# Optimization experiments

Measured on AMD Instinct MI355X. Metric: run time of the kernel, lower is better.

## Reference

```python
import jax, jax.numpy as jnp
import numpy as np

B, FEAT_DIM, GUIDE_DIM, NIR = 1, 128, 128, 33
HL, WL, HH, WH = 64, 64, 256, 256


def make_coord(h, w):
    # pixel-center coords in [-1,1], order (y, x) matching torch make_coord((h,w))
    ys = -1.0 + 1.0 / h + (2.0 / h) * jnp.arange(h, dtype=jnp.float32)
    xs = -1.0 + 1.0 / w + (2.0 / w) * jnp.arange(w, dtype=jnp.float32)
    yy, xx = jnp.meshgrid(ys, xs, indexing='ij')
    return jnp.stack([yy, xx], axis=-1)  # [h, w, 2]


def grid_sample_nearest(img, coord):
    # img [B,C,Hi,Wi]; coord [B,N,2] normalized (y,x).
    # Matches F.grid_sample(mode='nearest', align_corners=False, padding_mode='zeros')
    # (torch passes coord.flip(-1), i.e. (x,y); we index (y,x) directly -- equivalent).
    Bb, C, Hi, Wi = img.shape
    y, x = coord[..., 0], coord[..., 1]
    iy = jnp.round((y + 1.0) * Hi / 2.0 - 0.5).astype(jnp.int32)
    ix = jnp.round((x + 1.0) * Wi / 2.0 - 0.5).astype(jnp.int32)
    valid = (iy >= 0) & (iy < Hi) & (ix >= 0) & (ix < Wi)
    idx = jnp.clip(iy, 0, Hi - 1) * Wi + jnp.clip(ix, 0, Wi - 1)  # [B,N]
    g = jnp.take_along_axis(img.reshape(Bb, C, Hi * Wi), idx[:, None, :], axis=2)
    g = jnp.where(valid[:, None, :], g, 0.0)
    return jnp.transpose(g, (0, 2, 1))  # [B,N,C]


def depthwise3x3(x, k):
    C = x.shape[1]
    return jax.lax.conv_general_dilated(x, k[:, None, :, :], (1, 1), ((1, 1), (1, 1)),
                                        feature_group_count=C,
                                        dimension_numbers=('NCHW', 'OIHW', 'NCHW'))


def query_freq(feat, coord, hr_guide, mlp_fn):
    # local-ensemble implicit decode (query_freq_a / query_freq_p share this skeleton)
    b, c, h, w = feat.shape
    H, W = hr_guide.shape[-2], hr_guide.shape[-1]
    coord = jnp.broadcast_to(coord, (b, H * W, 2))
    fcoord = jnp.broadcast_to(jnp.transpose(make_coord(h, w), (2, 0, 1))[None], (b, 2, h, w))
    q_guide = grid_sample_nearest(hr_guide, coord)  # [b,N,Cg]
    rx, ry = 1.0 / h, 1.0 / w
    hw = jnp.array([float(h), float(w)], dtype=coord.dtype)
    preds = []
    for vx in (-1.0, 1.0):
        for vy in (-1.0, 1.0):
            c_ = coord + jnp.array([vx * rx, vy * ry], dtype=coord.dtype)
            q_feat = grid_sample_nearest(feat, c_)    # [b,N,Cf]
            q_coord = grid_sample_nearest(fcoord, c_)  # [b,N,2]
            rel = (coord - q_coord) * hw
            inp = jnp.concatenate([q_feat, q_guide, rel], axis=-1)  # [b,N,Cin]
            preds.append(mlp_fn(inp, H, W))  # [b,N,NIR]
    preds = jnp.stack(preds, axis=-1)  # [b,N,NIR,4]
    weight = jax.nn.softmax(preds[:, :, -1, :], axis=-1)  # [b,N,4]
    ret = jnp.sum(preds[:, :, :-1, :] * weight[:, :, None, :], axis=-1)  # [b,N,NIR-1]
    return jnp.transpose(ret, (0, 2, 1)).reshape(b, -1, H, W)


def fourier_unit(feat, coord, hr_guide, w1a, b1a, w2a, b2a, w3a, b3a,
                 pw1, dw1, pw2, dw2, pw3, dw3):
    def mlp_a(inp, H, W):  # plain MLP (imnet1)
        x = jax.nn.relu(inp @ w1a + b1a)
        x = jax.nn.relu(x @ w2a + b2a)
        return x @ w3a + b3a

    def mlp_p(inp, H, W):  # conv MLP (imnet2 / MLP_P)
        b = inp.shape[0]
        x = inp.reshape(b, -1, H, W)  # faithful to torch .view on [B,N,Cin]
        x = jax.nn.relu(depthwise3x3(jnp.einsum('bchw,oc->bohw', x, pw1), dw1))
        x = jax.nn.relu(depthwise3x3(jnp.einsum('bchw,oc->bohw', x, pw2), dw2))
        x = depthwise3x3(jnp.einsum('bchw,oc->bohw', x, pw3), dw3)
        return x.reshape(b, H * W, -1)  # faithful to torch .view(B,N,-1)

    feat_f = jnp.fft.fftn(feat, axes=(-2, -1))
    guide_f = jnp.fft.fftn(hr_guide, axes=(-2, -1))
    mag = query_freq(jnp.abs(feat_f), coord, jnp.abs(guide_f), mlp_a)
    pha = query_freq(jnp.angle(feat_f), coord, jnp.angle(guide_f), mlp_p)
    ffted = jax.lax.complex(mag * jnp.cos(pha), mag * jnp.sin(pha))
    return jnp.abs(jnp.fft.ifftn(ffted, axes=(-2, -1)))


def setup_inputs() -> dict:
    key = jax.random.key(0)
    ks = jax.random.split(key, 12)
    cin = FEAT_DIM + GUIDE_DIM + 2  # 258

    def lin(k, i, o):
        return jax.random.normal(k, (i, o), jnp.float32) / np.float32(np.sqrt(i))

    return dict(
        feat=jax.random.normal(ks[0], (B, FEAT_DIM, HL, WL), jnp.float32),
        coord=make_coord(HH, WH).reshape(1, HH * WH, 2),
        hr_guide=jax.random.normal(ks[1], (B, GUIDE_DIM, HH, WH), jnp.float32),
        w1a=lin(ks[2], cin, 256), b1a=jnp.zeros((256,), jnp.float32),
        w2a=lin(ks[3], 256, 128), b2a=jnp.zeros((128,), jnp.float32),
        w3a=lin(ks[4], 128, NIR), b3a=jnp.zeros((NIR,), jnp.float32),
        pw1=jax.random.normal(ks[5], (256, cin), jnp.float32) / np.float32(np.sqrt(cin)),
        dw1=jax.random.normal(ks[6], (256, 3, 3), jnp.float32) / np.float32(3.0),
        pw2=jax.random.normal(ks[7], (128, 256), jnp.float32) / np.float32(16.0),
        dw2=jax.random.normal(ks[8], (128, 3, 3), jnp.float32) / np.float32(3.0),
        pw3=jax.random.normal(ks[9], (NIR, 128), jnp.float32) / np.float32(np.sqrt(128.0)),
        dw3=jax.random.normal(ks[10], (NIR, 3, 3), jnp.float32) / np.float32(3.0),
    )


def reference(feat, coord, hr_guide, w1a, b1a, w2a, b2a, w3a, b3a,
              pw1, dw1, pw2, dw2, pw3, dw3):
    return fourier_unit(feat, coord, hr_guide, w1a, b1a, w2a, b2a, w3a, b3a,
                        pw1, dw1, pw2, dw2, pw3, dw3)
```

## Files before the change

kernel.cpp:

```cpp
#include <hip/hip_runtime.h>
#include <math.h>

typedef __attribute__((ext_vector_type(4))) float f32x4;
typedef __attribute__((ext_vector_type(8))) short bf16x8;
typedef _Float16 f16x8 __attribute__((ext_vector_type(8)));

__device__ __forceinline__ short f2bf(float v) {
    union { float f; unsigned u; } x; x.f = v;
    unsigned r = x.u + 0x7FFF + ((x.u >> 16) & 1);
    return (short)(r >> 16);
}
__device__ __forceinline__ float bf2f(short b) {
    union { unsigned u; float f; } x; x.u = ((unsigned)(unsigned short)b) << 16;
    return x.f;
}
__device__ __forceinline__ short f2h(float v) {
    union { _Float16 h; short s; } u; u.h = (_Float16)v; return u.s;
}
__device__ __forceinline__ void gload16(const void* g, void* l) {
    __builtin_amdgcn_global_load_lds((const __attribute__((address_space(1))) void*)g,
                                     (__attribute__((address_space(3))) void*)l, 16, 0, 0);
}

template<int N, int MODE>
__global__ __launch_bounds__(256)
void fft_lines(const float* __restrict__ in_real, const float* __restrict__ in_pha,
               const float2* __restrict__ in_c, float2* __restrict__ out_c,
               int nlines, int lpp, int plane_stride, int line_pitch, int stride,
               float sgn, float scale)
{
    constexpr int H = N / 2;
    constexpr int LPB = 256 / H;
    __shared__ float2 bufA[LPB][N];
    __shared__ float2 bufB[LPB][N];
    __shared__ float2 W[H];
    const int tid = threadIdx.x;
    const int sub = tid / H;
    const int b   = tid % H;
    const int L   = blockIdx.x * LPB + sub;
    if (tid < H) {
        float ang = (6.283185307179586f / N) * tid;
        float s, c; sincosf(ang, &s, &c);
        W[tid] = make_float2(c, sgn * s);
    }
    const bool active = (L < nlines);
    size_t base = 0;
    if (active) {
        int p = L / lpp, q = L - p * lpp;
        base = (size_t)p * plane_stride + (size_t)q * line_pitch;
        if (MODE == 0) {
            bufA[sub][b]     = make_float2(in_real[base + (size_t)b * stride], 0.f);
            bufA[sub][b + H] = make_float2(in_real[base + (size_t)(b + H) * stride], 0.f);
        } else if (MODE == 1) {
            bufA[sub][b]     = in_c[base + (size_t)b * stride];
            bufA[sub][b + H] = in_c[base + (size_t)(b + H) * stride];
        } else {
            float m0 = in_real[base + (size_t)b * stride];
            float p0 = in_pha [base + (size_t)b * stride];
            float m1 = in_real[base + (size_t)(b + H) * stride];
            float p1 = in_pha [base + (size_t)(b + H) * stride];
            float s0, c0, s1, c1;
            sincosf(p0, &s0, &c0);
            sincosf(p1, &s1, &c1);
            bufA[sub][b]     = make_float2(m0 * c0, m0 * s0);
            bufA[sub][b + H] = make_float2(m1 * c1, m1 * s1);
        }
    }
    __syncthreads();
    float2 (*X)[N] = bufA;
    float2 (*Y)[N] = bufB;
    int m = 1;
    #pragma unroll
    for (int l = H; l >= 1; l >>= 1) {
        int jm = b & ~(m - 1);
        float2 c0 = X[sub][b];
        float2 c1 = X[sub][b + H];
        float2 w  = W[jm];
        float2 s0 = make_float2(c0.x + c1.x, c0.y + c1.y);
        float2 d  = make_float2(c0.x - c1.x, c0.y - c1.y);
        float2 t  = make_float2(d.x * w.x - d.y * w.y, d.x * w.y + d.y * w.x);
        Y[sub][b + jm]     = s0;
        Y[sub][b + jm + m] = t;
        __syncthreads();
        float2 (*tmp)[N] = X; X = Y; Y = tmp;
        m <<= 1;
    }
    if (active) {
        float2 r0 = X[sub][b], r1 = X[sub][b + H];
        out_c[base + (size_t)b * stride]       = make_float2(r0.x * scale, r0.y * scale);
        out_c[base + (size_t)(b + H) * stride] = make_float2(r1.x * scale, r1.y * scale);
    }
}

template<int N, int TC, int ABSOUT>
__global__ __launch_bounds__(256)
void fft_cols(const float2* __restrict__ in, float2* __restrict__ outc,
              float* __restrict__ outr, float sgn, float scale)
{
    constexpr int Q     = N / 4;
    constexpr int LOG4  = (N == 64) ? 3 : 4;
    constexpr int PITCH = ((N + N / 8 - 8 + 31) / 32) * 32 + 8;
    constexpr int ELD   = (N * TC) / 256;
    constexpr int EBF   = (Q * TC) / 256;
    static_assert((Q * TC) % 256 == 0, "butterfly count must fill block");
    __shared__ float bRe[2][TC * PITCH];
    __shared__ float bIm[2][TC * PITCH];
    __shared__ float Wre[Q + Q / 8 + 1];
    __shared__ float Wim[Q + Q / 8 + 1];
    const int tid = threadIdx.x;
    const int plane = blockIdx.y;
    const int c0 = blockIdx.x * TC;
    const size_t pbase = (size_t)plane * N * N + c0;
    auto lidx = [](int cc, int row) { return cc * PITCH + row + (row >> 3); };

    if (tid < Q) {
        float ang = (6.283185307179586f / N) * tid;
        float s, c; sincosf(ang, &s, &c);
        int wi = tid + (tid >> 3);
        Wre[wi] = c; Wim[wi] = sgn * s;
    }
    #pragma unroll
    for (int e = 0; e < ELD; e++) {
        int q = tid + e * 256;
        int r = q / TC, cc = q % TC;
        float2 v = in[pbase + (size_t)r * N + cc];
        int li = lidx(cc, r);
        bRe[0][li] = v.x; bIm[0][li] = v.y;
    }
    __syncthreads();
    int cur = 0, m = 1;
    #pragma unroll
    for (int stage = 0; stage < LOG4; stage++) {
        #pragma unroll
        for (int e = 0; e < EBF; e++) {
            int idx = tid + e * 256;
            int b = idx % Q, cc = idx / Q;
            int jm = b & ~(m - 1);
            int base = 3 * jm + b;
            int i0 = lidx(cc, b),         i1 = lidx(cc, b + Q);
            int i2 = lidx(cc, b + 2 * Q), i3 = lidx(cc, b + 3 * Q);
            float x0r = bRe[cur][i0], x0i = bIm[cur][i0];
            float x1r = bRe[cur][i1], x1i = bIm[cur][i1];
            float x2r = bRe[cur][i2], x2i = bIm[cur][i2];
            float x3r = bRe[cur][i3], x3i = bIm[cur][i3];
            int wi = jm + (jm >> 3);
            float w1r = Wre[wi], w1i = Wim[wi];
            float w2r = w1r * w1r - w1i * w1i, w2i = 2.f * w1r * w1i;
            float w3r = w2r * w1r - w2i * w1i, w3i = w2r * w1i + w2i * w1r;
            float ar = x0r + x2r, ai = x0i + x2i;
            float br = x0r - x2r, bi = x0i - x2i;
            float cr = x1r + x3r, ci = x1i + x3i;
            float dr = x1r - x3r, di = x1i - x3i;
            float edr = -sgn * di, edi = sgn * dr;
            float y0r = ar + cr,  y0i = ai + ci;
            float y1r = br + edr, y1i = bi + edi;
            float y2r = ar - cr,  y2i = ai - ci;
            float y3r = br - edr, y3i = bi - edi;
            int o0 = lidx(cc, base),         o1 = lidx(cc, base + m);
            int o2 = lidx(cc, base + 2 * m), o3 = lidx(cc, base + 3 * m);
            bRe[cur ^ 1][o0] = y0r;                     bIm[cur ^ 1][o0] = y0i;
            bRe[cur ^ 1][o1] = y1r * w1r - y1i * w1i;   bIm[cur ^ 1][o1] = y1r * w1i + y1i * w1r;
            bRe[cur ^ 1][o2] = y2r * w2r - y2i * w2i;   bIm[cur ^ 1][o2] = y2r * w2i + y2i * w2r;
            bRe[cur ^ 1][o3] = y3r * w3r - y3i * w3i;   bIm[cur ^ 1][o3] = y3r * w3i + y3i * w3r;
        }
        __syncthreads();
        cur ^= 1; m <<= 2;
    }
    #pragma unroll
    for (int e = 0; e < ELD; e++) {
        int q = tid + e * 256;
        int r = q / TC, cc = q % TC;
        int li = lidx(cc, r);
        float vr = bRe[cur][li], vi = bIm[cur][li];
        if (ABSOUT) {
            outr[pbase + (size_t)r * N + cc] = scale * sqrtf(vr * vr + vi * vi);
        } else {
            outc[pbase + (size_t)r * N + cc] = make_float2(vr * scale, vi * scale);
        }
    }
}

__global__ __launch_bounds__(256)
void extract_t(const float2* __restrict__ Fc, short* __restrict__ fAbf,
               float* __restrict__ fPT)
{
    __shared__ float2 T[128][17];
    const int tid = threadIdx.x;
    const int o0 = blockIdx.x * 16;
    #pragma unroll
    for (int e = 0; e < 8; e++) {
        int q = tid + e * 256;
        int c = q >> 4, oo = q & 15;
        T[c][oo] = Fc[(size_t)c * 4096 + o0 + oo];
    }
    __syncthreads();
    #pragma unroll
    for (int e = 0; e < 8; e++) {
        int q = tid + e * 256;
        int oo = q >> 7, c = q & 127;
        float2 v = T[c][oo];
        size_t idx = (size_t)(o0 + oo) * 128 + c;
        fAbf[idx] = f2bf(sqrtf(v.x * v.x + v.y * v.y));
        fPT[idx]  = atan2f(v.y, v.x);
    }
}

__global__ __launch_bounds__(256)
void gbuild_t(const float2* __restrict__ E, short* __restrict__ Ga,
              float* __restrict__ Gpf)
{
    __shared__ float2 T[128][17];
    const int tid = threadIdx.x;
    const int n0 = blockIdx.x * 16;
    #pragma unroll
    for (int e = 0; e < 8; e++) {
        int q = tid + e * 256;
        int c = q >> 4, nn = q & 15;
        T[c][nn] = E[(size_t)c * 65536 + n0 + nn];
    }
    __syncthreads();
    #pragma unroll
    for (int e = 0; e < 8; e++) {
        int q = tid + e * 256;
        int nn = q >> 7, c = q & 127;
        float2 v = T[c][nn];
        size_t o = (size_t)(n0 + nn) * 128 + c;
        Ga[o]  = f2bf(sqrtf(v.x * v.x + v.y * v.y));
        Gpf[o] = atan2f(v.y, v.x);
    }
}

__global__ __launch_bounds__(256)
void mag_h1(const short* __restrict__ FA1, const short* __restrict__ H1g,
            const float* __restrict__ w1a, const float* __restrict__ b1a,
            short* __restrict__ h1, int vx, int vy)
{
    int t = blockIdx.x * 256 + threadIdx.x;
    int n = t >> 5, oc = (t & 31) * 8;
    int i = n >> 8, jx = n & 255;
    int iy = (2 * i + (vx < 0 ? -3 : 5)) >> 3;
    int ix = (2 * jx + (vy < 0 ? -3 : 5)) >> 3;
    bool valid = (iy >= 0 && iy < 64 && ix >= 0 && ix < 64);
    float ry = valid ? (0.5f * i - 2.f * iy - 0.75f) : (0.5f * i - 63.75f);
    float rx = valid ? (0.5f * jx - 2.f * ix - 0.75f) : (0.5f * jx - 63.75f);
    bf16x8 hv = *(const bf16x8*)&H1g[(size_t)n * 256 + oc];
    bf16x8 fv = {};
    if (valid) fv = *(const bf16x8*)&FA1[(size_t)(iy * 64 + ix) * 256 + oc];
    bf16x8 out;
    #pragma unroll
    for (int k = 0; k < 8; k++) {
        int o = oc + k;
        float v = b1a[o] + bf2f(hv[k]) + ry * w1a[128 * 256 + o] + rx * w1a[129 * 256 + o];
        if (valid) v += bf2f(fv[k]);
        out[k] = f2bf(fmaxf(v, 0.f));
    }
    *(bf16x8*)&h1[(size_t)n * 256 + oc] = out;
}

__global__ __launch_bounds__(256)
void bphase_tile(const float* __restrict__ featPT, const float* __restrict__ Gpf,
                 short* __restrict__ Xp, int vx, int vy)
{
    __shared__ short lds[64 * 146];
    const int tid = threadIdx.x;
    const int p0 = (blockIdx.x >> 1) * 64;
    const int half = blockIdx.x & 1;
    const int pl = tid & 63;
    const int p = p0 + pl;
    const int jq = tid >> 6;
    unsigned* out32 = (unsigned*)Xp;
    #pragma unroll 4
    for (int e = 0; e < 36; e++) {
        int jl = e * 4 + jq;
        int j = half * 144 + jl;
        float v = 0.f;
        if (j < 258) {
            unsigned f = (unsigned)j * 65536u + (unsigned)p;
            unsigned n = f / 258u;
            unsigned c = f - n * 258u;
            int i = (int)(n >> 8), jx = (int)(n & 255);
            int iy = (2 * i + (vx < 0 ? -3 : 5)) >> 3;
            int ix = (2 * jx + (vy < 0 ? -3 : 5)) >> 3;
            bool valid = (iy >= 0 && iy < 64 && ix >= 0 && ix < 64);
            if (c < 128u)       v = valid ? featPT[(size_t)(iy * 64 + ix) * 128 + c] : 0.f;
            else if (c < 256u)  v = Gpf[(size_t)n * 128 + (c - 128)];
            else if (c == 256u) v = valid ? (0.5f * i - 2.f * iy - 0.75f) : (0.5f * i - 63.75f);
            else                v = valid ? (0.5f * jx - 2.f * ix - 0.75f) : (0.5f * jx - 63.75f);
        }
        lds[pl * 146 + jl] = f2h(v);
    }
    __syncthreads();
    const unsigned* lds32 = (const unsigned*)lds;
    #pragma unroll 4
    for (int e = 0; e < 18; e++) {
        int idx = e * 256 + tid;
        int pw = idx / 72, dw = idx - pw * 72;
        out32[(size_t)(p0 + pw) * 144 + half * 72 + dw] = lds32[pw * 73 + dw];
    }
}

__global__ void wprep_T(const float* __restrict__ src, short* __restrict__ dst,
                        int Ncols, int Nd, int Kp, int k0, int kn, int kr0, int krn)
{
    int t = blockIdx.x * 256 + threadIdx.x;
    if (t >= Nd * Kp) return;
    int o = t / Kp, j = t - o * Kp;
    int c = (j < kn) ? (k0 + j) : ((j < kn + krn) ? (kr0 + j - kn) : -1);
    float v = 0.f;
    if (c >= 0 && o < Ncols) v = src[(size_t)c * Ncols + o];
    dst[t] = f2bf(v);
}
__global__ void wprep_f16(const float* __restrict__ src, short* __restrict__ dst,
                          int Nsrc, int Ksrc, int Nd, int Kp, int kn)
{
    int t = blockIdx.x * 256 + threadIdx.x;
    if (t >= Nd * Kp) return;
    int o = t / Kp, j = t - o * Kp;
    float v = 0.f;
    if (j < kn && o < Nsrc) v = src[(size_t)o * Ksrc + j];
    dst[t] = f2h(v);
}

template<int RELU, int BIAS, int CIN, int OUTT, int F16>
__global__ __launch_bounds__(256)
void gemm_mfma(const short* __restrict__ A, const short* __restrict__ Bt,
               const float* __restrict__ bias, const void* __restrict__ Cin,
               void* __restrict__ Cout,
               int K, int Apitch, int Bpitch, int ldc, int Nout)
{
    __shared__ short As[4096];
    __shared__ short Bs[4096];
    const int tid = threadIdx.x;
    const int wave = tid >> 6, lane = tid & 63;
    const int bm = blockIdx.y * 128, bn = blockIdx.x * 128;
    const int wr = wave >> 1, wc = wave & 1;
    const int srow = wave * 32 + (lane >> 2);
    const int scol = (lane & 3) * 8;
    const int ldsoff = srow * 32 + scol;
    f32x4 acc[4][4] = {};
    const int ks_n = K >> 5;
    for (int ks = 0; ks < ks_n; ks++) {
        const int k0 = ks << 5;
        const short* gA = A + (size_t)(bm + srow) * Apitch + k0 + scol;
        gload16(gA, &As[ldsoff]);
        gload16(gA + 16 * Apitch, &As[ldsoff + 512]);
        const short* gB = Bt + (size_t)(bn + srow) * Bpitch + k0 + scol;
        gload16(gB, &Bs[ldsoff]);
        gload16(gB + 16 * Bpitch, &Bs[ldsoff + 512]);
        __syncthreads();
        const int fr = lane & 15;
        const int kreg = (lane >> 4) << 3;
        bf16x8 ah[4], bh[4];
        #pragma unroll
        for (int m = 0; m < 4; m++)
            ah[m] = *(const bf16x8*)&As[(wr * 64 + m * 16 + fr) * 32 + kreg];
        #pragma unroll
        for (int n = 0; n < 4; n++)
            bh[n] = *(const bf16x8*)&Bs[(wc * 64 + n * 16 + fr) * 32 + kreg];
        #pragma unroll
        for (int m = 0; m < 4; m++)
            #pragma unroll
            for (int n = 0; n < 4; n++) {
                if constexpr (F16)
                    acc[m][n] = __builtin_amdgcn_mfma_f32_16x16x32_f16(
                        __builtin_bit_cast(f16x8, ah[m]),
                        __builtin_bit_cast(f16x8, bh[n]), acc[m][n], 0, 0, 0);
                else
                    acc[m][n] = __builtin_amdgcn_mfma_f32_16x16x32_bf16(
                        ah[m], bh[n], acc[m][n], 0, 0, 0);
            }
        __syncthreads();
    }
    const int fr = lane & 15;
    const int rg = (lane >> 4) * 4;
    #pragma unroll
    for (int n = 0; n < 4; n++) {
        const int col = bn + wc * 64 + n * 16 + fr;
        if (col >= Nout) continue;
        const float bv = BIAS ? bias[col] : 0.f;
        #pragma unroll
        for (int m = 0; m < 4; m++) {
            const int row0 = bm + wr * 64 + m * 16 + rg;
            #pragma unroll
            for (int r = 0; r < 4; r++) {
                float v = acc[m][n][r] + bv;
                const size_t ci = (size_t)(row0 + r) * ldc + col;
                if (CIN == 1) v += bf2f(((const short*)Cin)[ci]);
                if (RELU) v = fmaxf(v, 0.f);
                if constexpr (OUTT == 1)      ((float*)Cout)[ci] = v;
                else if constexpr (OUTT == 2) ((_Float16*)Cout)[ci] = (_Float16)v;
                else                          ((short*)Cout)[ci] = f2bf(v);
            }
        }
    }
}

template<int C, int RELU>
__global__ __launch_bounds__(256)
void dwconv_f16(const _Float16* __restrict__ in, const float* __restrict__ w,
                _Float16* __restrict__ out)
{
    constexpr int PX = 512 / C;
    const int tid = threadIdx.x;
    const int c = tid % C;
    const int sub = tid / C;
    const int p0 = blockIdx.x * PX + sub * 2;
    const int y = p0 >> 8, x0 = p0 & 255;
    float wk[9];
    #pragma unroll
    for (int k = 0; k < 9; k++) wk[k] = w[c * 9 + k];
    float v[3][4];
    #pragma unroll
    for (int dy = 0; dy < 3; dy++) {
        int yy = y + dy - 1;
        bool yv = (yy >= 0) && (yy <= 255);
        int yc = min(max(yy, 0), 255);
        #pragma unroll
        for (int dx = 0; dx < 4; dx++) {
            int xx = x0 + dx - 1;
            bool xv = (xx >= 0) && (xx <= 255);
            int xc = min(max(xx, 0), 255);
            float t = (float)in[(size_t)(yc * 256 + xc) * C + c];
            v[dy][dx] = (yv && xv) ? t : 0.f;
        }
    }
    float a0 = 0.f, a1 = 0.f;
    #pragma unroll
    for (int dy = 0; dy < 3; dy++)
        #pragma unroll
        for (int dx = 0; dx < 3; dx++) {
            a0 += v[dy][dx]     * wk[dy * 3 + dx];
            a1 += v[dy][dx + 1] * wk[dy * 3 + dx];
        }
    if (RELU) { a0 = fmaxf(a0, 0.f); a1 = fmaxf(a1, 0.f); }
    out[(size_t)p0 * C + c]       = (_Float16)a0;
    out[(size_t)(p0 + 1) * C + c] = (_Float16)a1;
}

__global__ __launch_bounds__(256)
void dwconv3_t(const float* __restrict__ in, const float* __restrict__ w,
               float* __restrict__ out)
{
    __shared__ float lds[33][65];
    const int tid = threadIdx.x;
    const int y = blockIdx.x >> 2;
    const int x0 = (blockIdx.x & 3) * 64;
    #pragma unroll
    for (int e = 0; e < 9; e++) {
        int q = e * 256 + tid;
        if (q < 2112) {
            int x = q / 33, c = q - x * 33;
            float acc = 0.f;
            #pragma unroll
            for (int dy = 0; dy < 3; dy++) {
                int yy = y + dy - 1;
                bool yv = (yy >= 0) && (yy <= 255);
                int yc = min(max(yy, 0), 255);
                #pragma unroll
                for (int dx = 0; dx < 3; dx++) {
                    int xx = x0 + x + dx - 1;
                    bool xv = (xx >= 0) && (xx <= 255);
                    int xc = min(max(xx, 0), 255);
                    float t = in[(size_t)(yc * 256 + xc) * 33 + c];
                    acc += ((yv && xv) ? t : 0.f) * w[c * 9 + dy * 3 + dx];
                }
            }
            lds[c][x] = acc;
        }
    }
    __syncthreads();
    const int xx = tid & 63, c4 = tid >> 6;
    #pragma unroll
    for (int cg = 0; cg < 36; cg += 4) {
        int cc = cg + c4;
        if (cc < 33)
            out[(size_t)cc * 65536 + y * 256 + x0 + xx] = lds[cc][xx];
    }
}

__global__ __launch_bounds__(256)
void ensemble_a(const short* __restrict__ P, float* __restrict__ mag)
{
    int n = blockIdx.x * 256 + threadIdx.x;
    float w[4]; float mx = -1e30f;
    #pragma unroll
    for (int s = 0; s < 4; s++) {
        w[s] = bf2f(P[((size_t)s * 65536 + n) * 33 + 32]);
        mx = fmaxf(mx, w[s]);
    }
    float sum = 0.f;
    #pragma unroll
    for (int s = 0; s < 4; s++) { w[s] = expf(w[s] - mx); sum += w[s]; }
    float inv = 1.f / sum;
    for (int ch = 0; ch < 32; ch++) {
        float a = 0.f;
        #pragma unroll
        for (int s = 0; s < 4; s++)
            a += bf2f(P[((size_t)s * 65536 + n) * 33 + ch]) * w[s];
        mag[(size_t)ch * 65536 + n] = a * inv;
    }
}

__global__ __launch_bounds__(256)
void ensemble_p(const float* __restrict__ P, float* __restrict__ pha)
{
    const size_t SOFF = (size_t)65536 * 33;
    int n = blockIdx.x * 256 + threadIdx.x;
    const size_t base = (size_t)n * 33;
    float w[4]; float mx = -1e30f;
    #pragma unroll
    for (int s = 0; s < 4; s++) {
        w[s] = P[(size_t)s * SOFF + base + 32];
        mx = fmaxf(mx, w[s]);
    }
    float sum = 0.f;
    #pragma unroll
    for (int s = 0; s < 4; s++) { w[s] = expf(w[s] - mx); sum += w[s]; }
    float inv = 1.f / sum;
    for (int jj = 0; jj < 32; jj++) {
        float a = 0.f;
        #pragma unroll
        for (int s = 0; s < 4; s++)
            a += P[(size_t)s * SOFF + base + jj] * w[s];
        pha[(size_t)jj * 65536 + n] = a * inv;
    }
}

extern "C" void kernel_launch(void* const* d_in, const int* in_sizes, int n_in,
                              void* d_out, int out_size, void* d_ws, size_t ws_size,
                              hipStream_t stream)
{
    (void)in_sizes; (void)n_in; (void)out_size; (void)ws_size;
    const float* feat = (const float*)d_in[0];
    const float* hr   = (const float*)d_in[2];
    const float* w1a  = (const float*)d_in[3];
    const float* b1a  = (const float*)d_in[4];
    const float* w2a  = (const float*)d_in[5];
    const float* b2a  = (const float*)d_in[6];
    const float* w3a  = (const float*)d_in[7];
    const float* b3a  = (const float*)d_in[8];
    const float* pw1  = (const float*)d_in[9];
    const float* dw1  = (const float*)d_in[10];
    const float* pw2  = (const float*)d_in[11];
    const float* dw2  = (const float*)d_in[12];
    const float* pw3  = (const float*)d_in[13];
    const float* dw3  = (const float*)d_in[14];

    char* W = (char*)d_ws;
    const size_t oA = 0;
    const size_t oB = 75497472;
    const size_t oC = oB + 67108864;
    const size_t oD = oC + 33554432;
    const size_t oM = oD + 34603008;
    const size_t oF = oM + 12582912;
    const size_t oN = oF + 786432;

    float2* E    = (float2*)(W + oA);
    short*  Xp   = (short*) (W + oA);
    _Float16* X2 = (_Float16*)(W + oA);
    short*  h1   = (short*) (W + oA + 20971520);
    float*  C3   = (float*) (W + oA);
    float*  Hp   = (float*) (W + oA);
    float2* Fc   = (float2*)(W + oB);
    short*  Ga   = (short*) (W + oB);
    short*  H1g  = (short*) (W + oB + 16777216);
    short*  h2   = (short*) (W + oB + 50331648);
    _Float16* C1 = (_Float16*)(W + oB);
    _Float16* C2 = (_Float16*)(W + oB);
    _Float16* X3 = (_Float16*)(W + oB + 33554432);
    float2* Z    = (float2*)(W + oB);
    float*  Gpf  = (float*) (W + oC);
    short*  PA   = (short*) (W + oD);
    float*  PP   = (float*) (W + oD);
    float*  featPT = (float*)(W + oM);
    float*  Hm     = (float*)(W + oM + 4194304);
    short* W1g = (short*)(W + oF + 81920);
    short* W2  = (short*)(W + oF + 147456);
    short* W3  = (short*)(W + oF + 212992);
    short* Pf  = (short*)(W + oF + 245760);
    short* P2  = (short*)(W + oF + 393216);
    short* P3  = (short*)(W + oF + 458752);
    short* W1a128 = (short*)(W + oF + 491520);
    short* featAbf = (short*)(W + oN);
    short* FA1     = (short*)(W + oN + 1048576);

    const size_t SOFF = (size_t)65536 * 33;

    wprep_T<<<128, 256, 0, stream>>>(w1a, W1a128, 256, 256, 128, 0, 128, 0, 0);
    wprep_T<<<128, 256, 0, stream>>>(w1a, W1g, 256, 256, 128, 128, 128, 0, 0);
    wprep_T<<<128, 256, 0, stream>>>(w2a, W2, 128, 128, 256, 0, 256, 0, 0);
    wprep_T<<<64,  256, 0, stream>>>(w3a, W3, 33, 128, 128, 0, 128, 0, 0);
    wprep_f16<<<288, 256, 0, stream>>>(pw1, Pf, 256, 258, 256, 288, 258);
    wprep_f16<<<128, 256, 0, stream>>>(pw2, P2, 128, 256, 128, 256, 256);
    wprep_f16<<<64,  256, 0, stream>>>(pw3, P3, 33, 128, 128, 128, 128);

    fft_lines<256, 0><<<16384, 256, 0, stream>>>(hr, nullptr, nullptr, E, 32768, 256, 65536, 256, 1, -1.f, 1.f);
    fft_cols<256, 8, 0><<<dim3(32, 128), 256, 0, stream>>>(E, E, nullptr, -1.f, 1.f);
    fft_lines<64, 0><<<1024, 256, 0, stream>>>(feat, nullptr, nullptr, Fc, 8192, 64, 4096, 64, 1, -1.f, 1.f);
    fft_cols<64, 16, 0><<<dim3(4, 128), 256, 0, stream>>>(Fc, Fc, nullptr, -1.f, 1.f);
    extract_t<<<256, 256, 0, stream>>>(Fc, featAbf, featPT);

    gbuild_t<<<4096, 256, 0, stream>>>(E, Ga, Gpf);

    gemm_mfma<0,0,0,0,0><<<dim3(2,512), 256, 0, stream>>>(Ga, W1g, nullptr, nullptr, H1g, 128, 128, 128, 256, 256);
    gemm_mfma<0,0,0,0,0><<<dim3(2,32), 256, 0, stream>>>(featAbf, W1a128, nullptr, nullptr, FA1, 128, 128, 128, 256, 256);

    for (int s = 0; s < 4; s++) {
        int vx = (s < 2) ? -1 : 1;
        int vy = (s & 1) ? 1 : -1;
        mag_h1<<<8192, 256, 0, stream>>>(FA1, H1g, w1a, b1a, h1, vx, vy);
        gemm_mfma<1,1,0,0,0><<<dim3(1,512), 256, 0, stream>>>(h1, W2, b2a, nullptr, h2, 256, 256, 256, 128, 128);
        gemm_mfma<0,1,0,0,0><<<dim3(1,512), 256, 0, stream>>>(h2, W3, b3a, nullptr, PA + (size_t)s * 65536 * 33, 128, 128, 128, 33, 33);
    }
    ensemble_a<<<256, 256, 0, stream>>>(PA, Hm);

    for (int s = 0; s < 4; s++) {
        int vx = (s < 2) ? -1 : 1;
        int vy = (s & 1) ? 1 : -1;
        bphase_tile<<<2048, 256, 0, stream>>>(featPT, Gpf, Xp, vx, vy);
        gemm_mfma<0,0,0,2,1><<<dim3(2,512), 256, 0, stream>>>(Xp, Pf, nullptr, nullptr, C1, 288, 288, 288, 256, 256);
        dwconv_f16<256,1><<<32768, 256, 0, stream>>>(C1, dw1, X2);
        gemm_mfma<0,0,0,2,1><<<dim3(1,512), 256, 0, stream>>>((const short*)X2, P2, nullptr, nullptr, C2, 256, 256, 256, 128, 128);
        dwconv_f16<128,1><<<16384, 256, 0, stream>>>(C2, dw2, X3);
        gemm_mfma<0,0,0,1,1><<<dim3(1,512), 256, 0, stream>>>((const short*)X3, P3, nullptr, nullptr, C3, 128, 128, 128, 33, 33);
        dwconv3_t<<<1024, 256, 0, stream>>>(C3, dw3, PP + (size_t)s * SOFF);
    }
    ensemble_p<<<256, 256, 0, stream>>>(PP, Hp);

    fft_lines<256, 2><<<4096, 256, 0, stream>>>(Hm, Hp, nullptr, Z, 8192, 256, 65536, 256, 1, 1.f, 1.f / 256.f);
    fft_cols<256, 8, 1><<<dim3(32, 32), 256, 0, stream>>>(Z, nullptr, (float*)d_out, 1.f, 1.f / 256.f);
}
```

Measured before the change: 838.3 us.

## Batch two ensemble shifts per launch in amplitude and phase pipelines

The four per-shift kernel chains now run as two iterations, each covering two shifts, with grids doubled and kernels deriving the shift from the block or pixel index. The aim is fewer launches and larger grids that fill the GPU better, cutting launch gaps and tail effects. Intermediate buffers are relaid out so they hold two shifts at once, which raises the working-set size and memory footprint and adds aliasing risk in the scratch buffer.

```diff
diff --git a/kernel.cpp b/kernel.cpp
--- a/kernel.cpp
+++ b/kernel.cpp
@@ -233,17 +233,21 @@
 __global__ __launch_bounds__(256)
 void mag_h1(const short* __restrict__ FA1, const short* __restrict__ H1g,
             const float* __restrict__ w1a, const float* __restrict__ b1a,
-            short* __restrict__ h1, int vx, int vy)
+            short* __restrict__ h1, int s0)
 {
     int t = blockIdx.x * 256 + threadIdx.x;
     int n = t >> 5, oc = (t & 31) * 8;
-    int i = n >> 8, jx = n & 255;
-    int iy = (2 * i + (vx < 0 ? -3 : 5)) >> 3;
-    int ix = (2 * jx + (vy < 0 ? -3 : 5)) >> 3;
+    int im = n >> 16, nl = n & 65535;
+    int s = s0 + im;
+    int oy = (s < 2) ? -3 : 5;
+    int ox = (s & 1) ? 5 : -3;
+    int i = nl >> 8, jx = nl & 255;
+    int iy = (2 * i + oy) >> 3;
+    int ix = (2 * jx + ox) >> 3;
     bool valid = (iy >= 0 && iy < 64 && ix >= 0 && ix < 64);
     float ry = valid ? (0.5f * i - 2.f * iy - 0.75f) : (0.5f * i - 63.75f);
     float rx = valid ? (0.5f * jx - 2.f * ix - 0.75f) : (0.5f * jx - 63.75f);
-    bf16x8 hv = *(const bf16x8*)&H1g[(size_t)n * 256 + oc];
+    bf16x8 hv = *(const bf16x8*)&H1g[(size_t)nl * 256 + oc];
     bf16x8 fv = {};
     if (valid) fv = *(const bf16x8*)&FA1[(size_t)(iy * 64 + ix) * 256 + oc];
     bf16x8 out;
@@ -259,16 +263,21 @@
 
 __global__ __launch_bounds__(256)
 void bphase_tile(const float* __restrict__ featPT, const float* __restrict__ Gpf,
-                 short* __restrict__ Xp, int vx, int vy)
+                 short* __restrict__ Xp, int s0)
 {
     __shared__ short lds[64 * 146];
     const int tid = threadIdx.x;
-    const int p0 = (blockIdx.x >> 1) * 64;
-    const int half = blockIdx.x & 1;
+    const int sh = blockIdx.x >> 11;
+    const int inner = blockIdx.x & 2047;
+    const int s = s0 + sh;
+    const int oy = (s < 2) ? -3 : 5;
+    const int ox = (s & 1) ? 5 : -3;
+    const int p0 = (inner >> 1) * 64;
+    const int half = inner & 1;
     const int pl = tid & 63;
     const int p = p0 + pl;
     const int jq = tid >> 6;
-    unsigned* out32 = (unsigned*)Xp;
+    unsigned* out32 = (unsigned*)Xp + (size_t)sh * 65536 * 144;
     #pragma unroll 4
     for (int e = 0; e < 36; e++) {
         int jl = e * 4 + jq;
@@ -279,8 +288,8 @@
             unsigned n = f / 258u;
             unsigned c = f - n * 258u;
             int i = (int)(n >> 8), jx = (int)(n & 255);
-            int iy = (2 * i + (vx < 0 ? -3 : 5)) >> 3;
-            int ix = (2 * jx + (vy < 0 ? -3 : 5)) >> 3;
+            int iy = (2 * i + oy) >> 3;
+            int ix = (2 * jx + ox) >> 3;
             bool valid = (iy >= 0 && iy < 64 && ix >= 0 && ix < 64);
             if (c < 128u)       v = valid ? featPT[(size_t)(iy * 64 + ix) * 128 + c] : 0.f;
             else if (c < 256u)  v = Gpf[(size_t)n * 128 + (c - 128)];
@@ -405,7 +414,10 @@
     const int c = tid % C;
     const int sub = tid / C;
     const int p0 = blockIdx.x * PX + sub * 2;
-    const int y = p0 >> 8, x0 = p0 & 255;
+    const int im = p0 >> 16;
+    const int pl = p0 & 65535;
+    const int y = pl >> 8, x0 = pl & 255;
+    const size_t ibase = (size_t)im * 65536 * C;
     float wk[9];
     #pragma unroll
     for (int k = 0; k < 9; k++) wk[k] = w[c * 9 + k];
@@ -420,7 +432,7 @@
             int xx = x0 + dx - 1;
             bool xv = (xx >= 0) && (xx <= 255);
             int xc = min(max(xx, 0), 255);
-            float t = (float)in[(size_t)(yc * 256 + xc) * C + c];
+            float t = (float)in[ibase + (size_t)(yc * 256 + xc) * C + c];
             v[dy][dx] = (yv && xv) ? t : 0.f;
         }
     }
@@ -443,8 +455,12 @@
 {
     __shared__ float lds[33][65];
     const int tid = threadIdx.x;
-    const int y = blockIdx.x >> 2;
-    const int x0 = (blockIdx.x & 3) * 64;
+    const int im = blockIdx.x >> 10;
+    const int inner = blockIdx.x & 1023;
+    const int y = inner >> 2;
+    const int x0 = (inner & 3) * 64;
+    const size_t ibase = (size_t)im * 65536 * 33;
+    const size_t obase = (size_t)im * 65536 * 33;
     #pragma unroll
     for (int e = 0; e < 9; e++) {
         int q = e * 256 + tid;
@@ -461,7 +477,7 @@
                     int xx = x0 + x + dx - 1;
                     bool xv = (xx >= 0) && (xx <= 255);
                     int xc = min(max(xx, 0), 255);
-                    float t = in[(size_t)(yc * 256 + xc) * 33 + c];
+                    float t = in[ibase + (size_t)(yc * 256 + xc) * 33 + c];
                     acc += ((yv && xv) ? t : 0.f) * w[c * 9 + dy * 3 + dx];
                 }
             }
@@ -474,7 +490,7 @@
     for (int cg = 0; cg < 36; cg += 4) {
         int cc = cg + c4;
         if (cc < 33)
-            out[(size_t)cc * 65536 + y * 256 + x0 + xx] = lds[cc][xx];
+            out[obase + (size_t)cc * 65536 + y * 256 + x0 + xx] = lds[cc][xx];
     }
 }
 
@@ -555,23 +571,23 @@
     const size_t oF = oM + 12582912;
     const size_t oN = oF + 786432;
 
-    float2* E    = (float2*)(W + oA);
-    short*  Xp   = (short*) (W + oA);
-    _Float16* X2 = (_Float16*)(W + oA);
-    short*  h1   = (short*) (W + oA + 20971520);
-    float*  C3   = (float*) (W + oA);
-    float*  Hp   = (float*) (W + oA);
-    float2* Fc   = (float2*)(W + oB);
-    short*  Ga   = (short*) (W + oB);
-    short*  H1g  = (short*) (W + oB + 16777216);
-    short*  h2   = (short*) (W + oB + 50331648);
-    _Float16* C1 = (_Float16*)(W + oB);
-    _Float16* C2 = (_Float16*)(W + oB);
-    _Float16* X3 = (_Float16*)(W + oB + 33554432);
-    float2* Z    = (float2*)(W + oB);
-    float*  Gpf  = (float*) (W + oC);
-    short*  PA   = (short*) (W + oD);
-    float*  PP   = (float*) (W + oD);
+    float2* E     = (float2*)(W + oA);
+    short*  h1_2  = (short*) (W + oA);
+    short*  Xp2   = (short*) (W + oA);
+    _Float16* X2_2 = (_Float16*)(W + oA);
+    float*  C3_2  = (float*) (W + oA);
+    float*  Hp    = (float*) (W + oA);
+    float2* Fc    = (float2*)(W + oB);
+    short*  Ga    = (short*) (W + oB);
+    short*  h2_2  = (short*) (W + oB);
+    short*  H1g   = (short*) (W + oB + 33554432);
+    _Float16* C1_2 = (_Float16*)(W + oB);
+    _Float16* C2_2 = (_Float16*)(W + oB);
+    _Float16* X3_2 = (_Float16*)(W + oB + 33554432);
+    float2* Z     = (float2*)(W + oB);
+    float*  Gpf   = (float*) (W + oC);
+    short*  PA    = (short*) (W + oD);
+    float*  PP    = (float*) (W + oD);
     float*  featPT = (float*)(W + oM);
     float*  Hm     = (float*)(W + oM + 4194304);
     short* W1g = (short*)(W + oF + 81920);
@@ -605,25 +621,21 @@
     gemm_mfma<0,0,0,0,0><<<dim3(2,512), 256, 0, stream>>>(Ga, W1g, nullptr, nullptr, H1g, 128, 128, 128, 256, 256);
     gemm_mfma<0,0,0,0,0><<<dim3(2,32), 256, 0, stream>>>(featAbf, W1a128, nullptr, nullptr, FA1, 128, 128, 128, 256, 256);
 
-    for (int s = 0; s < 4; s++) {
-        int vx = (s < 2) ? -1 : 1;
-        int vy = (s & 1) ? 1 : -1;
-        mag_h1<<<8192, 256, 0, stream>>>(FA1, H1g, w1a, b1a, h1, vx, vy);
-        gemm_mfma<1,1,0,0,0><<<dim3(1,512), 256, 0, stream>>>(h1, W2, b2a, nullptr, h2, 256, 256, 256, 128, 128);
-        gemm_mfma<0,1,0,0,0><<<dim3(1,512), 256, 0, stream>>>(h2, W3, b3a, nullptr, PA + (size_t)s * 65536 * 33, 128, 128, 128, 33, 33);
+    for (int s0 = 0; s0 < 4; s0 += 2) {
+        mag_h1<<<16384, 256, 0, stream>>>(FA1, H1g, w1a, b1a, h1_2, s0);
+        gemm_mfma<1,1,0,0,0><<<dim3(1,1024), 256, 0, stream>>>(h1_2, W2, b2a, nullptr, h2_2, 256, 256, 256, 128, 128);
+        gemm_mfma<0,1,0,0,0><<<dim3(1,1024), 256, 0, stream>>>(h2_2, W3, b3a, nullptr, PA + (size_t)s0 * SOFF, 128, 128, 128, 33, 33);
     }
     ensemble_a<<<256, 256, 0, stream>>>(PA, Hm);
 
-    for (int s = 0; s < 4; s++) {
-        int vx = (s < 2) ? -1 : 1;
-        int vy = (s & 1) ? 1 : -1;
-        bphase_tile<<<2048, 256, 0, stream>>>(featPT, Gpf, Xp, vx, vy);
-        gemm_mfma<0,0,0,2,1><<<dim3(2,512), 256, 0, stream>>>(Xp, Pf, nullptr, nullptr, C1, 288, 288, 288, 256, 256);
-        dwconv_f16<256,1><<<32768, 256, 0, stream>>>(C1, dw1, X2);
-        gemm_mfma<0,0,0,2,1><<<dim3(1,512), 256, 0, stream>>>((const short*)X2, P2, nullptr, nullptr, C2, 256, 256, 256, 128, 128);
-        dwconv_f16<128,1><<<16384, 256, 0, stream>>>(C2, dw2, X3);
-        gemm_mfma<0,0,0,1,1><<<dim3(1,512), 256, 0, stream>>>((const short*)X3, P3, nullptr, nullptr, C3, 128, 128, 128, 33, 33);
-        dwconv3_t<<<1024, 256, 0, stream>>>(C3, dw3, PP + (size_t)s * SOFF);
+    for (int s0 = 0; s0 < 4; s0 += 2) {
+        bphase_tile<<<4096, 256, 0, stream>>>(featPT, Gpf, Xp2, s0);
+        gemm_mfma<0,0,0,2,1><<<dim3(2,1024), 256, 0, stream>>>(Xp2, Pf, nullptr, nullptr, C1_2, 288, 288, 288, 256, 256);
+        dwconv_f16<256,1><<<65536, 256, 0, stream>>>(C1_2, dw1, X2_2);
+        gemm_mfma<0,0,0,2,1><<<dim3(1,1024), 256, 0, stream>>>((const short*)X2_2, P2, nullptr, nullptr, C2_2, 256, 256, 256, 128, 128);
+        dwconv_f16<128,1><<<32768, 256, 0, stream>>>(C2_2, dw2, X3_2);
+        gemm_mfma<0,0,0,1,1><<<dim3(1,1024), 256, 0, stream>>>((const short*)X3_2, P3, nullptr, nullptr, C3_2, 128, 128, 128, 33, 33);
+        dwconv3_t<<<2048, 256, 0, stream>>>(C3_2, dw3, PP + (size_t)s0 * SOFF);
     }
     ensemble_p<<<256, 256, 0, stream>>>(PP, Hp);
 
```

After: 790.5 us. 1.06x faster.
